# Kernel tuning notes

Hardware: AMD Instinct MI355X
Metric: run time of the kernel (lower is better)

The kernel has to match this reference:

```python
import jax, jax.numpy as jnp
import numpy as np

# ---- module config (mirrors arch_args / init_kwargs) ----
W_BITS_PER_SLICE = 4      # slice_init=True -> weights quantized with STE to w_bits_per_slice
A_BITS = 8                # activation quantization bits
A_BITS_PER_STREAM = 8
VMAX = 1.0
GON_HW, GOFF_HW = 1.0, 1e-3   # weight_to_diff_conductance is called with Gon=1, Goff=1/1000 (hardcoded)
ADC_PREC = 8
ADC_STEP = 1e-3           # adc_static_step
NUM_SUBARRAYS = 9
SUB_SIZE = 256            # subarray_size; 256*3*3 / 256 = 9 even chunks
K, STRIDE, PAD = 3, 1, 1


def ste_quantize(x, bits):
    # Symmetric uniform quantizer with straight-through estimator (STE_Quantize).
    n = float(2 ** bits - 1)
    s = jnp.max(jnp.abs(x)) + 1e-12
    q = jnp.round(x / s * n) / n * s
    return x + jax.lax.stop_gradient(q - x)


def adc_quantize(I):
    # Nbit_ADC: static-step uniform ADC, signed (adc_pos_only=False), deterministic
    # rounding (adc_stoch_round=False), STE backward, no custom loss.
    half = 2 ** (ADC_PREC - 1)
    q = jnp.clip(jnp.round(I / ADC_STEP), -half, half - 1) * ADC_STEP
    return I + jax.lax.stop_gradient(q - I)


def setup_inputs():
    key = jax.random.key(0)
    k1, k2 = jax.random.split(key)
    x = jax.random.normal(k1, (32, 256, 32, 32), jnp.float32)
    fan_in = 256 * K * K
    w = jax.random.normal(k2, (256, 256, K, K), jnp.float32) * np.sqrt(2.0 / fan_in)  # kaiming_normal
    return {"inputs": x, "weight": w}


def reference(inputs, weight):
    B = inputs.shape[0]
    O = weight.shape[0]

    # forward(): quantize activations (a_bits) and weights (w_bits_per_slice, slice_init path)
    qa = ste_quantize(inputs, A_BITS)
    qw = ste_quantize(weight, W_BITS_PER_SLICE)

    # F.unfold -> [B, C*k*k, L], channel-major patch ordering (matches torch)
    patches = jax.lax.conv_general_dilated_patches(
        qa, (K, K), (STRIDE, STRIDE), ((PAD, PAD), (PAD, PAD)))
    Hp, Wp = patches.shape[2], patches.shape[3]
    L = Hp * Wp
    V = patches.reshape(B, NUM_SUBARRAYS, SUB_SIZE, L) * (VMAX / A_BITS_PER_STREAM)

    # Differential conductances: G_pos - G_neg. The dummy columns (both filled with
    # Goff) cancel exactly in I_pos - I_neg, so the net current per subarray is a
    # single contraction against qw * (Gon - Goff) / Nstates_slice.
    nstates = float(2 ** W_BITS_PER_SLICE - 1)
    Gd = qw.reshape(O, NUM_SUBARRAYS, SUB_SIZE) * ((GON_HW - GOFF_HW) / nstates)

    # per-subarray crossbar currents: [B, n_sub, O, L]
    I = jnp.einsum('bgfl,ogf->bgol', V, Gd)

    # shared ADC applied to each subarray output, then accumulate over subarrays
    accum = adc_quantize(I).sum(axis=1)  # [B, O, L]
    a_loss = jnp.float32(0.0)            # adc_custom_loss=False

    # F.fold with (1,1) kernel onto sqrt(L) x sqrt(L) grid == reshape
    result = accum.reshape(B, O, Hp, Wp)
    return (result, a_loss)
```

## Files before the change

kernel.cpp:

```cpp
#include <hip/hip_runtime.h>
#include <stdint.h>

typedef unsigned short u16;
typedef __attribute__((ext_vector_type(8))) short short8;
typedef __attribute__((ext_vector_type(4))) float floatx4;

#define NB 32
#define NC 256
#define NH 32
#define NW 32
#define NO 256
#define NPIX (NH*NW)
#define KPIX 9
#define NG 9
#define RUN 32
#define GK (NG*RUN)
#define KTOT (NG*GK)
#define PADH 34
#define PADSP (PADH*PADH)
#define QA_BSTRIDE (PADSP*NC)

#define AS1 __attribute__((address_space(1)))
#define AS3 __attribute__((address_space(3)))

__global__ void fused_pre(const float4* __restrict__ x4, int nx4,
                          const float4* __restrict__ w4, int nw4,
                          float* __restrict__ pmax, u16* __restrict__ qa) {
  int bid = blockIdx.x;
  if (bid >= 1088) {
    int zb = bid - 1088;
    int b = zb / 9;
    int rem = (zb % 9) * 256 + threadIdx.x;
    if (rem >= 2112) return;
    int pb = rem >> 4, c16 = rem & 15;
    int y, x;
    if (pb < 68) { y = (pb >= 34) ? 33 : 0; x = pb % 34; }
    else { int q = pb - 68; y = 1 + (q >> 1); x = (q & 1) ? 33 : 0; }
    uint4 z; z.x = z.y = z.z = z.w = 0u;
    *(uint4*)(qa + ((size_t)(b * PADH + y) * PADH + x) * NC + c16 * 16) = z;
    return;
  }
  const float4* p; int n4; int nb, b0;
  if (bid < 1024) { p = x4; n4 = nx4; nb = 1024; b0 = bid; }
  else            { p = w4; n4 = nw4; nb = 64;   b0 = bid - 1024; }
  float m = 0.f;
  for (int i = b0 * blockDim.x + threadIdx.x; i < n4; i += nb * blockDim.x) {
    float4 v = p[i];
    m = fmaxf(m, fmaxf(fmaxf(fabsf(v.x), fabsf(v.y)), fmaxf(fabsf(v.z), fabsf(v.w))));
  }
#pragma unroll
  for (int off = 32; off > 0; off >>= 1)
    m = fmaxf(m, __shfl_down(m, off, 64));
  __shared__ float sm[4];
  int lane = threadIdx.x & 63, wv = threadIdx.x >> 6;
  if (lane == 0) sm[wv] = m;
  __syncthreads();
  if (threadIdx.x == 0)
    pmax[bid] = fmaxf(fmaxf(sm[0], sm[1]), fmaxf(sm[2], sm[3]));
}

__device__ inline void reduce_pmax(const float* pmax, int tid, int nthreads,
                                   float* sred, float& mx_out, float& mw_out) {
  const float4* pf4 = (const float4*)pmax;
  float mx = 0.f, mw = 0.f;
  for (int t = tid; t < 256; t += nthreads) {
    float4 v = pf4[t];
    mx = fmaxf(mx, fmaxf(fmaxf(v.x, v.y), fmaxf(v.z, v.w)));
  }
  if (tid < 16) {
    float4 v = pf4[256 + tid];
    mw = fmaxf(fmaxf(v.x, v.y), fmaxf(v.z, v.w));
  }
#pragma unroll
  for (int off = 32; off > 0; off >>= 1) {
    mx = fmaxf(mx, __shfl_down(mx, off, 64));
    mw = fmaxf(mw, __shfl_down(mw, off, 64));
  }
  int lane = tid & 63, wv = tid >> 6, nw = nthreads >> 6;
  if (lane == 0) { sred[wv] = mx; sred[8 + wv] = mw; }
  __syncthreads();
  mx = sred[0]; mw = sred[8];
  for (int i = 1; i < nw; i++) { mx = fmaxf(mx, sred[i]); mw = fmaxf(mw, sred[8 + i]); }
  mx_out = mx; mw_out = mw;
}

__global__ void fused_quant(const float* __restrict__ x, const float* __restrict__ w,
                            const float* __restrict__ pmax,
                            u16* __restrict__ qa, u16* __restrict__ wq,
                            float* __restrict__ lossp) {
  __shared__ float sred[16];
  float mx, mw;
  reduce_pmax(pmax, threadIdx.x, 256, sred, mx, mw);
  int bid = blockIdx.x, tid = threadIdx.x;
  if (bid < 1024) {
    __shared__ u16 ts[32][264];
    double s = (double)mx + 1e-12;
    double inv = 255.0 / s;
    int b = bid >> 5, y = bid & 31;
    const float4* x4 = (const float4*)x;
    int xc = tid & 7, crow = tid >> 3;
#pragma unroll
    for (int it = 0; it < 8; it++) {
      int c = crow + 32 * it;
      float4 v = x4[((size_t)(b * NC + c) * NH + y) * 8 + xc];
      float q0 = (float)rint((double)v.x * inv);
      float q1 = (float)rint((double)v.y * inv);
      float q2 = (float)rint((double)v.z * inv);
      float q3 = (float)rint((double)v.w * inv);
      ts[xc * 4 + 0][c] = (u16)(__float_as_uint(q0) >> 16);
      ts[xc * 4 + 1][c] = (u16)(__float_as_uint(q1) >> 16);
      ts[xc * 4 + 2][c] = (u16)(__float_as_uint(q2) >> 16);
      ts[xc * 4 + 3][c] = (u16)(__float_as_uint(q3) >> 16);
    }
    __syncthreads();
    int xx = tid >> 3, qwl = tid & 7;
    u16* orow = qa + ((size_t)(b * PADH + y + 1) * PADH + (xx + 1)) * NC;
#pragma unroll
    for (int it = 0; it < 4; it++) {
      int qw = qwl + 8 * it;
      *(uint4*)(orow + qw * 8) = *(const uint4*)&ts[xx][qw * 8];
    }
    return;
  }
  double s = (double)mw + 1e-12;
  double inv = 15.0 / s;
  int idx = (bid - 1024) * 256 + tid;
  if (idx == 0) *lossp = 0.0f;
  int o = idx / KTOT, kk = idx % KTOT;
  int g = kk / GK, rem = kk % GK;
  int r = rem / RUN, j = rem % RUN;
  int clo = (256 * g - r + 8) / 9;
  int chi = (256 * (g + 1) - r + 8) / 9; if (chi > NC) chi = NC;
  int cst = ((256 * g) / 9) & ~3;
  int c = cst + j;
  float val = 0.f;
  if (c >= clo && c < chi) {
    float wv = w[((size_t)o * NC + c) * KPIX + r];
    val = (float)rint((double)wv * inv);
  }
  wq[idx] = (u16)(__float_as_uint(val) >> 16);
}

__global__ __launch_bounds__(256, 2) void gemm_adc(const u16* __restrict__ qa,
                                                   const u16* __restrict__ wq,
                                                   const float* __restrict__ pmax,
                                                   float* __restrict__ out) {
  __shared__ __align__(16) u16 lB[12288];
  __shared__ __align__(16) u16 sA[6528];
  __shared__ float sred[16];
  const int tid = threadIdx.x;
  float mx, mw;
  reduce_pmax(pmax, tid, 256, sred, mx, mw);

  const int mblk = blockIdx.x, nblk = blockIdx.y;
  const int b = mblk >> 3;
  const int p0 = (mblk & 7) * 128;
  const int y0 = (mblk & 7) * 4;
  const int n0 = nblk * 128;
  const int lane = tid & 63, wv = tid >> 6;
  const int wm = (wv & 1) * 64, wn = (wv >> 1) * 64;
  const int fm = lane & 15, fq = lane >> 4;
  const int swz = (fq + ((fm >> 1) & 3)) & 3;

  double sa = (double)mx + 1e-12;
  double sw = (double)mw + 1e-12;
  double Sstep = sa * sw * 0.999 / 459.0;

  const int OFS[9] = {0, 1, 2, 34, 35, 36, 68, 69, 70};
  int addrA[4][9];
#pragma unroll
  for (int mi = 0; mi < 4; mi++) {
    int pr = wm + mi * 16 + fm;
    int pixb = (pr >> 5) * 34 + (pr & 31);
#pragma unroll
    for (int t = 0; t < 9; t++) {
      int P = pixb + OFS[t];
      addrA[mi][t] = P * 32 + (((fq + ((P >> 1) & 3)) & 3) << 3);
    }
  }
  int bno[4];
#pragma unroll
  for (int ni = 0; ni < 4; ni++) bno[ni] = (wn + ni * 16 + fm) * RUN + swz * 8;

  const int r0 = tid >> 2;
  const int jsrc = ((tid & 3) - ((tid >> 3) & 3)) & 3;
  const u16* BbH[2];
#pragma unroll
  for (int h = 0; h < 2; h++)
    BbH[h] = wq + (size_t)(n0 + r0 + 64 * h) * KTOT + jsrc * 8;

  const u16* Abase = qa + (size_t)b * QA_BSTRIDE + (size_t)y0 * PADH * NC;
  const bool sact = tid < 204;
  int soff[4], sdst[4];
#pragma unroll
  for (int i = 0; i < 4; i++) {
    int s = i * 204 + tid;
    soff[i] = (s >> 2) * NC + ((((s & 3) - ((s >> 3) & 3)) & 3) << 3);
    sdst[i] = s * 8;
  }

  floatx4 acc[4][4];
  float tot[4][4][4];
#pragma unroll
  for (int mi = 0; mi < 4; mi++)
#pragma unroll
    for (int ni = 0; ni < 4; ni++)
#pragma unroll
      for (int rr = 0; rr < 4; rr++) { acc[mi][ni][rr] = 0.f; tot[mi][ni][rr] = 0.f; }

#pragma unroll 1
  for (int g = 0; g < NG; g++) {
    int cw = ((256 * g) / 9) & ~3;
    if (sact) {
      const u16* srcg = Abase + cw;
#pragma unroll
      for (int i = 0; i < 4; i++)
        __builtin_amdgcn_global_load_lds((const AS1 void*)(srcg + soff[i]),
                                         (AS3 void*)&sA[sdst[i]], 16, 0, 0);
    }
    {
      int kb0 = g * GK;
#pragma unroll
      for (int i = 0; i < 6; i++)
        __builtin_amdgcn_global_load_lds((const AS1 void*)(BbH[i & 1] + kb0 + (i >> 1) * RUN),
                                         (AS3 void*)&lB[(tid + 256 * i) * 8], 16, 0, 0);
    }
    if (g > 0) {
#pragma unroll
      for (int mi = 0; mi < 4; mi++)
#pragma unroll
        for (int ni = 0; ni < 4; ni++)
#pragma unroll
          for (int rr = 0; rr < 4; rr++) {
            double d = (double)acc[mi][ni][rr] * Sstep;
            float tf = (float)rint(d);
            tf = fminf(fmaxf(tf, -128.f), 127.f);
            tot[mi][ni][rr] += tf;
            acc[mi][ni][rr] = 0.f;
          }
    }
#pragma unroll
    for (int rc = 0; rc < 3; rc++) {
      __syncthreads();
#pragma unroll
      for (int ri = 0; ri < 3; ri++) {
        short8 afr[4], bfr[4];
#pragma unroll
        for (int mi = 0; mi < 4; mi++)
          afr[mi] = *(const short8*)&sA[addrA[mi][rc * 3 + ri]];
#pragma unroll
        for (int ni = 0; ni < 4; ni++)
          bfr[ni] = *(const short8*)&lB[ri * 4096 + bno[ni]];
#pragma unroll
        for (int mi = 0; mi < 4; mi++)
#pragma unroll
          for (int ni = 0; ni < 4; ni++)
            acc[mi][ni] = __builtin_amdgcn_mfma_f32_16x16x32_bf16(afr[mi], bfr[ni], acc[mi][ni], 0, 0, 0);
      }
      __syncthreads();
      if (rc < 2) {
        int kb0 = g * GK + (rc + 1) * 3 * RUN;
#pragma unroll
        for (int i = 0; i < 6; i++)
          __builtin_amdgcn_global_load_lds((const AS1 void*)(BbH[i & 1] + kb0 + (i >> 1) * RUN),
                                           (AS3 void*)&lB[(tid + 256 * i) * 8], 16, 0, 0);
      }
    }
  }
#pragma unroll
  for (int mi = 0; mi < 4; mi++)
#pragma unroll
    for (int ni = 0; ni < 4; ni++)
#pragma unroll
      for (int rr = 0; rr < 4; rr++) {
        double d = (double)acc[mi][ni][rr] * Sstep;
        float tf = (float)rint(d);
        tf = fminf(fmaxf(tf, -128.f), 127.f);
        tot[mi][ni][rr] += tf;
      }

#pragma unroll
  for (int mi = 0; mi < 4; mi++)
#pragma unroll
    for (int ni = 0; ni < 4; ni++) {
      int o = n0 + wn + ni * 16 + fm;
      int p = p0 + wm + mi * 16 + fq * 4;
      float4 o4;
      o4.x = tot[mi][ni][0] * 1e-3f;
      o4.y = tot[mi][ni][1] * 1e-3f;
      o4.z = tot[mi][ni][2] * 1e-3f;
      o4.w = tot[mi][ni][3] * 1e-3f;
      *(float4*)(out + ((size_t)(b * NO + o)) * NPIX + p) = o4;
    }
}

extern "C" void kernel_launch(void* const* d_in, const int* in_sizes, int n_in,
                              void* d_out, int out_size, void* d_ws, size_t ws_size,
                              hipStream_t stream) {
  const float* x = (const float*)d_in[0];
  const float* w = (const float*)d_in[1];
  float* out = (float*)d_out;

  float* pmax = (float*)d_ws;
  u16* qa = (u16*)((char*)d_ws + 8192);
  u16* wq = (u16*)((char*)d_ws + 8192 + 18939904 + 8192);

  fused_pre<<<1376, 256, 0, stream>>>((const float4*)x, (NB * NC * NH * NW) / 4,
                                      (const float4*)w, (NO * NC * KPIX) / 4,
                                      pmax, qa);
  fused_quant<<<1024 + 2592, 256, 0, stream>>>(x, w, pmax, qa, wq, out + (out_size - 1));
  gemm_adc<<<dim3(256, 2), 256, 0, stream>>>(qa, wq, pmax, out);
}
```

Baseline: 146.8 us.

## Double-buffer A slab and B tiles in LDS to overlap loads with MFMA

Doubles the LDS buffers for the activation slab and the weight tiles. The next group's slab and the next B chunk are issued before computing on the current buffers, which removes one barrier per chunk and hides global-to-LDS latency behind MFMA work. LDS use roughly doubles, to about 75 KB per block, which may cut occupancy below the two blocks per CU requested in launch bounds. Correctness relies on the single barrier per chunk ordering the async LDS writes against reads of the other buffer.

Measured after the change: 162.6 us. 1.11x slower.

```diff
diff --git a/kernel.cpp b/kernel.cpp
--- a/kernel.cpp
+++ b/kernel.cpp
@@ -145,8 +145,8 @@
                                                    const u16* __restrict__ wq,
                                                    const float* __restrict__ pmax,
                                                    float* __restrict__ out) {
-  __shared__ __align__(16) u16 lB[12288];
-  __shared__ __align__(16) u16 sA[6528];
+  __shared__ __align__(16) u16 lB[24576];
+  __shared__ __align__(16) u16 sA[13056];
   __shared__ float sred[16];
   const int tid = threadIdx.x;
   float mx, mw;
@@ -208,49 +208,66 @@
 #pragma unroll
       for (int rr = 0; rr < 4; rr++) { acc[mi][ni][rr] = 0.f; tot[mi][ni][rr] = 0.f; }
 
+  auto STAGE_SLAB = [&](int gp) {
+    int cw = ((256 * gp) / 9) & ~3;
+    int ad = (gp & 1) * 6528;
+    if (sact) {
+      const u16* srcg = Abase + cw;
+#pragma unroll
+      for (int i = 0; i < 4; i++)
+        __builtin_amdgcn_global_load_lds((const AS1 void*)(srcg + soff[i]),
+                                         (AS3 void*)&sA[ad + sdst[i]], 16, 0, 0);
+    }
+  };
+  auto STAGE_B = [&](int kb0, int bbn) {
+#pragma unroll
+    for (int i = 0; i < 6; i++)
+      __builtin_amdgcn_global_load_lds((const AS1 void*)(BbH[i & 1] + kb0 + (i >> 1) * RUN),
+                                       (AS3 void*)&lB[bbn + (tid + 256 * i) * 8], 16, 0, 0);
+  };
+  auto FOLD = [&]() {
+#pragma unroll
+    for (int mi = 0; mi < 4; mi++)
+#pragma unroll
+      for (int ni = 0; ni < 4; ni++)
+#pragma unroll
+        for (int rr = 0; rr < 4; rr++) {
+          double d = (double)acc[mi][ni][rr] * Sstep;
+          float tf = (float)rint(d);
+          tf = fminf(fmaxf(tf, -128.f), 127.f);
+          tot[mi][ni][rr] += tf;
+          acc[mi][ni][rr] = 0.f;
+        }
+  };
+
+  STAGE_SLAB(0);
+  STAGE_B(0, 0);
+  __syncthreads();
+
 #pragma unroll 1
   for (int g = 0; g < NG; g++) {
-    int cw = ((256 * g) / 9) & ~3;
-    if (sact) {
-      const u16* srcg = Abase + cw;
-#pragma unroll
-      for (int i = 0; i < 4; i++)
-        __builtin_amdgcn_global_load_lds((const AS1 void*)(srcg + soff[i]),
-                                         (AS3 void*)&sA[sdst[i]], 16, 0, 0);
-    }
-    {
-      int kb0 = g * GK;
-#pragma unroll
-      for (int i = 0; i < 6; i++)
-        __builtin_amdgcn_global_load_lds((const AS1 void*)(BbH[i & 1] + kb0 + (i >> 1) * RUN),
-                                         (AS3 void*)&lB[(tid + 256 * i) * 8], 16, 0, 0);
-    }
-    if (g > 0) {
-#pragma unroll
-      for (int mi = 0; mi < 4; mi++)
-#pragma unroll
-        for (int ni = 0; ni < 4; ni++)
-#pragma unroll
-          for (int rr = 0; rr < 4; rr++) {
-            double d = (double)acc[mi][ni][rr] * Sstep;
-            float tf = (float)rint(d);
-            tf = fminf(fmaxf(tf, -128.f), 127.f);
-            tot[mi][ni][rr] += tf;
-            acc[mi][ni][rr] = 0.f;
-          }
-    }
+    const int ab = (g & 1) * 6528;
 #pragma unroll
     for (int rc = 0; rc < 3; rc++) {
-      __syncthreads();
+      if (!(g == 8 && rc == 2)) {
+        int kb0 = (rc == 2) ? (g + 1) * GK : g * GK + (rc + 1) * 96;
+        int bbn = ((g + rc + 1) & 1) * 12288;
+        STAGE_B(kb0, bbn);
+      }
+      if (rc == 0) {
+        if (g < 8) STAGE_SLAB(g + 1);
+        if (g > 0) FOLD();
+      }
+      const int bb = ((g + rc) & 1) * 12288;
 #pragma unroll
       for (int ri = 0; ri < 3; ri++) {
         short8 afr[4], bfr[4];
 #pragma unroll
         for (int mi = 0; mi < 4; mi++)
-          afr[mi] = *(const short8*)&sA[addrA[mi][rc * 3 + ri]];
+          afr[mi] = *(const short8*)&sA[ab + addrA[mi][rc * 3 + ri]];
 #pragma unroll
         for (int ni = 0; ni < 4; ni++)
-          bfr[ni] = *(const short8*)&lB[ri * 4096 + bno[ni]];
+          bfr[ni] = *(const short8*)&lB[bb + ri * 4096 + bno[ni]];
 #pragma unroll
         for (int mi = 0; mi < 4; mi++)
 #pragma unroll
@@ -258,13 +275,6 @@
             acc[mi][ni] = __builtin_amdgcn_mfma_f32_16x16x32_bf16(afr[mi], bfr[ni], acc[mi][ni], 0, 0, 0);
       }
       __syncthreads();
-      if (rc < 2) {
-        int kb0 = g * GK + (rc + 1) * 3 * RUN;
-#pragma unroll
-        for (int i = 0; i < 6; i++)
-          __builtin_amdgcn_global_load_lds((const AS1 void*)(BbH[i & 1] + kb0 + (i >> 1) * RUN),
-                                           (AS3 void*)&lB[(tid + 256 * i) * 8], 16, 0, 0);
-      }
     }
   }
 #pragma unroll
```
